# Kernel optimization log

Measured on AMD Instinct MI355X. Metric: run time of the kernel, lower is better.

The kernel has to match this reference:

```python
import jax, jax.numpy as jnp
import numpy as np

R0 = 1.0
DIM_A, DIM_V, DIM_D = 32, 32, 32
N_NODES = 20000
N_EDGES = 640000


def radial_encode_8(r, r0):
    # 8 Gaussian radial basis functions on the edge length |r_ij|
    d = jnp.linalg.norm(r, axis=-1)                      # [E]
    centers = jnp.linspace(0.0, r0, 8)                   # [8]
    width = r0 / 8.0
    return jnp.exp(-(((d[..., None] - centers) / width) ** 2))  # [E,8]


def tens_sigmoid_vec(v):
    # norm-saturating nonlinearity for rank-1 tensors (direction-preserving)
    n2 = jnp.sum(v * v, axis=-1, keepdims=True)
    return v * jax.lax.rsqrt(1.0 + n2)


def setup_inputs() -> dict:
    key = jax.random.key(0)
    ks = jax.random.split(key, 12)

    def lin(k, fan_in, fan_out):
        return jax.random.normal(k, (fan_in, fan_out), jnp.float32) / np.float32(np.sqrt(fan_in))

    return dict(
        r_ij=jax.random.normal(ks[0], (N_EDGES, 3), jnp.float32),
        w_rad=lin(ks[1], 8, DIM_A), b_rad=jnp.zeros((DIM_A,), jnp.float32),
        w_direct=lin(ks[2], DIM_A, DIM_A),
        w1=lin(ks[3], DIM_A, 2 * DIM_A), b1=jnp.zeros((2 * DIM_A,), jnp.float32),
        w2=lin(ks[4], 2 * DIM_A, 2 * DIM_A), b2=jnp.zeros((2 * DIM_A,), jnp.float32),
        w3=lin(ks[5], 2 * DIM_A, DIM_A), b3=jnp.zeros((DIM_A,), jnp.float32),
        w_v=lin(ks[6], DIM_A, DIM_V),
        w_d=lin(ks[7], DIM_A, DIM_D),
        edges_src=jax.random.randint(ks[8], (N_EDGES,), 0, N_NODES),
        n_nodes=N_NODES,
    )


def reference(r_ij, w_rad, b_rad, w_direct, w1, b1, w2, b2, w3, b3, w_v, w_d,
              edges_src, n_nodes):
    lrelu = lambda x: jnp.where(x > 0, x, 0.1 * x)
    # radial MLP: Linear(8, a) -> MLP (lin_direct + 3-layer leakyrelu net)
    h = radial_encode_8(r_ij, R0) @ w_rad + b_rad                      # [E,a]
    rad = h @ w_direct + (lrelu(lrelu(h @ w1 + b1) @ w2 + b2) @ w3 + b3)  # [E,a]
    rs = tens_sigmoid_vec(r_ij * (7.0 / R0))                            # [E,3]

    seg = lambda x: jax.ops.segment_sum(x, edges_src, num_segments=n_nodes)
    A_a = seg(rad)                                                      # [N,a]
    A_v = seg(rad[:, :, None] * rs[:, None, :])                         # [N,a,3]
    # phi_d_ij = rad ⊗ rs ⊗ rs per edge  -> [E,a,3,3], then scatter-sum
    A_d = seg(rad[:, :, None, None] * rs[:, None, None, :] * rs[:, None, :, None])  # [N,a,3,3]

    out_v = jnp.einsum('nac,av->nvc', A_v, w_v)                         # TensLinear rank 1
    out_d = jnp.einsum('naij,ad->ndij', A_d, w_d)                       # TensLinear rank 2
    return A_a, out_v, out_d
```

## Files before the change

### kernel.cpp

```cpp
#include <hip/hip_runtime.h>
#include <hip/hip_bf16.h>
#include <hip/hip_fp16.h>
#include <math.h>


#define TSIZE 8192
#define DMAX  2.0f
#define EPB   4
#define NPB   4
#define ROWB  512
#define ROWF  128

#define O_WRAD 0
#define O_BRAD 256
#define O_WDIR 288
#define O_W1   1312
#define O_B1   3360
#define O_W2   3424
#define O_B2   7520
#define O_W3   7584
#define O_B3   9632
#define O_WV   9664
#define O_WD   10688
#define W_TOT  11712

typedef float        f32x4 __attribute__((ext_vector_type(4)));
typedef unsigned int u32x2 __attribute__((ext_vector_type(2)));

struct TE { float r, v, d; };

__device__ __forceinline__ float lrelu(float x) { return x > 0.0f ? x : 0.1f * x; }

__device__ __forceinline__ float ldf(const void* p, int i, bool f32) {
    return f32 ? ((const float*)p)[i]
               : __uint_as_float(((unsigned int)((const unsigned short*)p)[i]) << 16);
}
__device__ __forceinline__ void stf(void* p, size_t i, float v, bool f32) {
    if (f32) ((float*)p)[i] = v;
    else     ((__hip_bfloat16*)p)[i] = __float2bfloat16(v);
}

__device__ __forceinline__ bool detect_f32(const void* r) {
    const unsigned short* p = (const unsigned short*)r;
    int bad = 0;
#pragma unroll 8
    for (int i = 0; i < 128; i++) {
        float v = __uint_as_float(((unsigned int)p[i]) << 16);
        bad |= (!isfinite(v) || fabsf(v) > 1e5f) ? 1 : 0;
    }
    return bad != 0;
}

__device__ __forceinline__ void load8x16(
    const void* p0, const void* p1, const void* p2, const void* p3,
    const void* p4, const void* p5, const void* p6, const void* p7,
    f32x4& q0, f32x4& q1, f32x4& q2, f32x4& q3,
    f32x4& q4, f32x4& q5, f32x4& q6, f32x4& q7) {
    asm volatile(
        "global_load_dwordx4 %0, %8, off\n\t"
        "global_load_dwordx4 %1, %9, off\n\t"
        "global_load_dwordx4 %2, %10, off\n\t"
        "global_load_dwordx4 %3, %11, off\n\t"
        "global_load_dwordx4 %4, %12, off\n\t"
        "global_load_dwordx4 %5, %13, off\n\t"
        "global_load_dwordx4 %6, %14, off\n\t"
        "global_load_dwordx4 %7, %15, off\n\t"
        "s_waitcnt vmcnt(0)"
        : "=&v"(q0), "=&v"(q1), "=&v"(q2), "=&v"(q3),
          "=&v"(q4), "=&v"(q5), "=&v"(q6), "=&v"(q7)
        : "v"(p0), "v"(p1), "v"(p2), "v"(p3),
          "v"(p4), "v"(p5), "v"(p6), "v"(p7));
}

__global__ void __launch_bounds__(256) k_prep(
    const void* __restrict__ r_ij,
    const void* w_rad, const void* b_rad, const void* w_direct,
    const void* w1, const void* b1, const void* w2, const void* b2,
    const void* w3, const void* b3, const void* w_v, const void* w_d,
    float* __restrict__ wcat, int* __restrict__ flag,
    int* __restrict__ counts, int N) {
    const int b = blockIdx.x;
    if (b == 0) {
        if (threadIdx.x == 0) flag[0] = detect_f32(r_ij) ? 1 : 0;
    } else if (b <= 11) {
        const bool f32 = detect_f32(r_ij);
        const void* src; int cnt; int off;
        switch (b) {
            case 1:  src = w_rad;    cnt = 256;  off = O_WRAD; break;
            case 2:  src = b_rad;    cnt = 32;   off = O_BRAD; break;
            case 3:  src = w_direct; cnt = 1024; off = O_WDIR; break;
            case 4:  src = w1;       cnt = 2048; off = O_W1;   break;
            case 5:  src = b1;       cnt = 64;   off = O_B1;   break;
            case 6:  src = w2;       cnt = 4096; off = O_W2;   break;
            case 7:  src = b2;       cnt = 64;   off = O_B2;   break;
            case 8:  src = w3;       cnt = 2048; off = O_W3;   break;
            case 9:  src = b3;       cnt = 32;   off = O_B3;   break;
            case 10: src = w_v;      cnt = 1024; off = O_WV;   break;
            default: src = w_d;      cnt = 1024; off = O_WD;   break;
        }
        for (int i = threadIdx.x; i < cnt; i += 256)
            wcat[off + i] = ldf(src, i, f32);
    } else {
        const int i = (b - 12) * 256 + threadIdx.x;
        if (i < N) counts[i] = 0;
    }
}

__global__ void __launch_bounds__(64 * EPB) k_tabrank(
    const float* __restrict__ wcat, float* __restrict__ tabI,
    const int* __restrict__ src, int* __restrict__ counts,
    unsigned short* __restrict__ rank, int E) {
    __shared__ float Lh[EPB][32], Lt1[EPB][64], Lt2[EPB][64], Lrad[EPB][32];

    const int TB = TSIZE / EPB;
    if (blockIdx.x >= TB) {
        const int e = (blockIdx.x - TB) * 256 + threadIdx.x;
        if (e < E) rank[e] = (unsigned short)atomicAdd(&counts[src[e]], 1);
        return;
    }

    const int s = threadIdx.x >> 6;
    const int j = threadIdx.x & 63;
    const int e = blockIdx.x * EPB + s;
    const float d = (float)e * (DMAX / (float)(TSIZE - 1));

    float enc[8];
#pragma unroll
    for (int k = 0; k < 8; k++) {
        float t = (d - (float)k * (1.0f / 7.0f)) * 8.0f;
        enc[k] = expf(-t * t);
    }

    if (j < 32) {
        float hv = wcat[O_BRAD + j];
#pragma unroll
        for (int k = 0; k < 8; k++) hv = fmaf(enc[k], wcat[O_WRAD + k * 32 + j], hv);
        Lh[s][j] = hv;
    }
    __syncthreads();

    {
        float v = wcat[O_B1 + j];
#pragma unroll
        for (int i = 0; i < 32; i++) v = fmaf(Lh[s][i], wcat[O_W1 + i * 64 + j], v);
        Lt1[s][j] = lrelu(v);
    }
    __syncthreads();

    {
        float v = wcat[O_B2 + j];
#pragma unroll
        for (int i = 0; i < 64; i++) v = fmaf(Lt1[s][i], wcat[O_W2 + i * 64 + j], v);
        Lt2[s][j] = lrelu(v);
    }
    __syncthreads();

    if (j < 32) {
        float v = wcat[O_B3 + j];
#pragma unroll
        for (int i = 0; i < 64; i++) v = fmaf(Lt2[s][i], wcat[O_W3 + i * 32 + j], v);
#pragma unroll
        for (int i = 0; i < 32; i++) v = fmaf(Lh[s][i], wcat[O_WDIR + i * 32 + j], v);
        Lrad[s][j] = v;
    }
    __syncthreads();

    if (j < 32) {
        float sv = 0.0f, sd = 0.0f;
#pragma unroll
        for (int i = 0; i < 32; i++) {
            float ri = Lrad[s][i];
            sv = fmaf(ri, wcat[O_WV + i * 32 + j], sv);
            sd = fmaf(ri, wcat[O_WD + i * 32 + j], sd);
        }
        float* row = tabI + (size_t)e * ROWF + j * 4;
        row[0] = Lrad[s][j];
        row[1] = sv;
        row[2] = sd;
        row[3] = 0.0f;
    }
}

__global__ void __launch_bounds__(1024) k_scan(const int* __restrict__ counts,
                                               int* __restrict__ rowstart,
                                               int N, int E) {
    __shared__ int part[1024];
    const int t = threadIdx.x;
    const int CH = (N + 1023) / 1024;
    const int lo = t * CH;
    const int hi = min(lo + CH, N);
    int s = 0;
    for (int i = lo; i < hi; i++) s += counts[i];
    part[t] = s;
    __syncthreads();
    for (int off = 1; off < 1024; off <<= 1) {
        int v = part[t];
        int w = (t >= off) ? part[t - off] : 0;
        __syncthreads();
        part[t] = v + w;
        __syncthreads();
    }
    int run = (t == 0) ? 0 : part[t - 1];
    for (int i = lo; i < hi; i++) { rowstart[i] = run; run += counts[i]; }
    if (t == 0) rowstart[N] = E;
}

template <bool P16>
__global__ void __launch_bounds__(256) k_place2(
        const int* __restrict__ src, const unsigned short* __restrict__ rank,
        const int* __restrict__ rowstart, const void* __restrict__ r_ij,
        const int* __restrict__ flag, void* __restrict__ epsv, int E) {
    const bool f32 = flag[0] != 0;
    const int e = blockIdx.x * 256 + threadIdx.x;
    if (e >= E) return;
    const int pos = rowstart[src[e]] + (int)rank[e];
    const float x = ldf(r_ij, 3 * e + 0, f32);
    const float y = ldf(r_ij, 3 * e + 1, f32);
    const float z = ldf(r_ij, 3 * e + 2, f32);
    const float d2 = x * x + y * y + z * z;
    const float inv = rsqrtf(1.0f + 49.0f * d2);
    const float u = fminf(sqrtf(d2), DMAX) * ((float)(TSIZE - 1) / DMAX);
    const int ti = (int)(u + 0.5f);
    const float rs0 = 7.0f * x * inv, rs1 = 7.0f * y * inv, rs2 = 7.0f * z * inv;
    if (P16) {
        ((float4*)epsv)[pos] =
            make_float4(rs0, rs1, rs2, __int_as_float(ti * ROWB));
    } else {
        const unsigned int h0 = __half_as_ushort(__float2half(rs0));
        const unsigned int h1 = __half_as_ushort(__float2half(rs1));
        const unsigned int h2 = __half_as_ushort(__float2half(rs2));
        ((uint2*)epsv)[pos] =
            make_uint2(h0 | (h1 << 16), h2 | ((unsigned)ti << 16));
    }
}

#define ACC16(Q, U)                                                           \
    do {                                                                      \
        const float x = (Q).x, y = (Q).y, z = (Q).z;                          \
        accA += (U).x;                                                        \
        v0 += (U).y * x; v1 += (U).y * y; v2 += (U).y * z;                    \
        const float _tx = (U).z * x, _ty = (U).z * y, _tz = (U).z * z;        \
        d00 += _tx * x; d01 += _tx * y; d02 += _tx * z;                       \
        d10 += _ty * x; d11 += _ty * y; d12 += _ty * z;                       \
        d20 += _tz * x; d21 += _tz * y; d22 += _tz * z;                       \
    } while (0)

template <bool P16>
__global__ void __launch_bounds__(64 * NPB, 4) k_nodes2(
    const void* __restrict__ epsv,
    const int* __restrict__ rowstart,
    const float* __restrict__ tabI,
    const int* __restrict__ flag,
    void* __restrict__ out, int N) {
    const int wave = threadIdx.x >> 6;
    const int lane = threadIdx.x & 63;
    const int n0 = (blockIdx.x * NPB + wave) * 2;
    const int a = lane & 31;
    const int half = lane >> 5;
    const int myn = n0 + half;
    const bool f32 = flag[0] != 0;
    const char* tabA = (const char*)tabI + a * 16;

    int s0 = 0, s1 = 0;
    if (myn < N) { s0 = rowstart[myn]; s1 = rowstart[myn + 1]; }
    const int mylen = s1 - s0;
    const int lenA = __shfl(mylen, 0);
    const int lenB = __shfl(mylen, 32);
    const int minl = min(lenA, lenB);
    const int maxl = max(lenA, lenB);
    const int mclamp = max(mylen - 1, 0);

    float accA = 0.f, v0 = 0.f, v1 = 0.f, v2 = 0.f;
    float d00 = 0.f, d01 = 0.f, d02 = 0.f,
          d10 = 0.f, d11 = 0.f, d12 = 0.f,
          d20 = 0.f, d21 = 0.f, d22 = 0.f;

    if (P16) {
        int i = 0;
        for (; i + 8 <= minl; i += 8) {
            const char* pb = (const char*)epsv + (size_t)(s0 + i) * 16;
            f32x4 q0, q1, q2, q3, q4, q5, q6, q7;
            load8x16(pb, pb + 16, pb + 32, pb + 48,
                     pb + 64, pb + 80, pb + 96, pb + 112,
                     q0, q1, q2, q3, q4, q5, q6, q7);
            f32x4 u0, u1, u2, u3, u4, u5, u6, u7;
            load8x16(tabA + __float_as_int(q0.w), tabA + __float_as_int(q1.w),
                     tabA + __float_as_int(q2.w), tabA + __float_as_int(q3.w),
                     tabA + __float_as_int(q4.w), tabA + __float_as_int(q5.w),
                     tabA + __float_as_int(q6.w), tabA + __float_as_int(q7.w),
                     u0, u1, u2, u3, u4, u5, u6, u7);
            ACC16(q0, u0); ACC16(q1, u1); ACC16(q2, u2); ACC16(q3, u3);
            ACC16(q4, u4); ACC16(q5, u5); ACC16(q6, u6); ACC16(q7, u7);
        }
        for (; i < maxl; i += 8) {
            float m0, m1, m2, m3, m4, m5, m6, m7;
#define TIDX(K) ((i + K) < mylen ? (i + K) : mclamp)
#define TPTR(K) ((const char*)epsv + (size_t)(s0 + TIDX(K)) * 16)
            m0 = (i + 0 < mylen) ? 1.f : 0.f;
            m1 = (i + 1 < mylen) ? 1.f : 0.f;
            m2 = (i + 2 < mylen) ? 1.f : 0.f;
            m3 = (i + 3 < mylen) ? 1.f : 0.f;
            m4 = (i + 4 < mylen) ? 1.f : 0.f;
            m5 = (i + 5 < mylen) ? 1.f : 0.f;
            m6 = (i + 6 < mylen) ? 1.f : 0.f;
            m7 = (i + 7 < mylen) ? 1.f : 0.f;
            f32x4 q0, q1, q2, q3, q4, q5, q6, q7;
            load8x16(TPTR(0), TPTR(1), TPTR(2), TPTR(3),
                     TPTR(4), TPTR(5), TPTR(6), TPTR(7),
                     q0, q1, q2, q3, q4, q5, q6, q7);
#undef TPTR
#undef TIDX
            f32x4 u0, u1, u2, u3, u4, u5, u6, u7;
            load8x16(tabA + __float_as_int(q0.w), tabA + __float_as_int(q1.w),
                     tabA + __float_as_int(q2.w), tabA + __float_as_int(q3.w),
                     tabA + __float_as_int(q4.w), tabA + __float_as_int(q5.w),
                     tabA + __float_as_int(q6.w), tabA + __float_as_int(q7.w),
                     u0, u1, u2, u3, u4, u5, u6, u7);
#define SAPX(K)                                                               \
            do { f32x4 uu = u##K; uu.x *= m##K; uu.y *= m##K; uu.z *= m##K;   \
                 ACC16(q##K, uu); } while (0)
            SAPX(0); SAPX(1); SAPX(2); SAPX(3);
            SAPX(4); SAPX(5); SAPX(6); SAPX(7);
#undef SAPX
        }
    } else {
        for (int i = 0; i < maxl; i++) {
            if (i < mylen) {
                const u32x2 qh = *((const u32x2*)epsv + (s0 + i));
                const float x = __half2float(__ushort_as_half(
                    (unsigned short)(qh.x & 0xffffu)));
                const float y = __half2float(__ushort_as_half(
                    (unsigned short)(qh.x >> 16)));
                const float z = __half2float(__ushort_as_half(
                    (unsigned short)(qh.y & 0xffffu)));
                const TE t = *(const TE*)(tabA + (int)(qh.y >> 16) * ROWB);
                accA += t.r;
                v0 += t.v * x; v1 += t.v * y; v2 += t.v * z;
                const float _tx = t.d * x, _ty = t.d * y, _tz = t.d * z;
                d00 += _tx * x; d01 += _tx * y; d02 += _tx * z;
                d10 += _ty * x; d11 += _ty * y; d12 += _ty * z;
                d20 += _tz * x; d21 += _tz * y; d22 += _tz * z;
            }
        }
    }

    if (myn >= N) return;
    const size_t baseV = (size_t)N * 32;
    const size_t baseD = (size_t)N * 128;
    stf(out, (size_t)myn * 32 + a, accA, f32);
    const size_t vb = baseV + (size_t)myn * 96 + a * 3;
    stf(out, vb + 0, v0, f32);
    stf(out, vb + 1, v1, f32);
    stf(out, vb + 2, v2, f32);
    const size_t db = baseD + (size_t)myn * 288 + a * 9;
    stf(out, db + 0, d00, f32);
    stf(out, db + 1, d01, f32);
    stf(out, db + 2, d02, f32);
    stf(out, db + 3, d10, f32);
    stf(out, db + 4, d11, f32);
    stf(out, db + 5, d12, f32);
    stf(out, db + 6, d20, f32);
    stf(out, db + 7, d21, f32);
    stf(out, db + 8, d22, f32);
}

__global__ void __launch_bounds__(256) k_place_g(
        const int* __restrict__ src, const unsigned short* __restrict__ rank,
        const int* __restrict__ rowstart, int* __restrict__ perm, int E) {
    const int e = blockIdx.x * 256 + threadIdx.x;
    if (e < E) perm[rowstart[src[e]] + (int)rank[e]] = e;
}
__global__ void __launch_bounds__(256) k_nodes_fb(
    const int* __restrict__ perm, const void* __restrict__ r_ij,
    const int* __restrict__ rowstart, const float* __restrict__ tabI,
    const int* __restrict__ flag, void* __restrict__ out, int N) {
    const int wave = threadIdx.x >> 6;
    const int lane = threadIdx.x & 63;
    const int n = blockIdx.x * 4 + wave;
    if (n >= N) return;
    const int a = lane & 31;
    const bool hi = (lane >> 5) != 0;
    const bool f32 = flag[0] != 0;
    const int s0 = rowstart[n], s1 = rowstart[n + 1];
    float accR = 0.f, acc1 = 0.f, acc2 = 0.f, acc3 = 0.f,
          acc4 = 0.f, acc5 = 0.f, acc6 = 0.f;
    for (int idx = s0; idx < s1; idx++) {
        const int e = perm[idx];
        const float x0 = ldf(r_ij, 3 * e + 0, f32);
        const float y0 = ldf(r_ij, 3 * e + 1, f32);
        const float z0 = ldf(r_ij, 3 * e + 2, f32);
        const float d2 = x0 * x0 + y0 * y0 + z0 * z0;
        const float inv = rsqrtf(1.0f + 49.0f * d2);
        const float x = 7.0f * x0 * inv, y = 7.0f * y0 * inv, z = 7.0f * z0 * inv;
        const float u = fminf(sqrtf(d2), DMAX) * ((float)(TSIZE - 1) / DMAX);
        const int b = (int)(u + 0.5f) * ROWF + a * 4;
        const float ra = tabI[b], rv = tabI[b + 1], rd = tabI[b + 2];
        const float b1 = (hi ? rd : rv) * (hi ? y : 1.0f);
        const float b2 = rd * (hi ? z : x);
        accR += ra;
        acc1 += b1 * x; acc2 += b1 * y; acc3 += b1 * z;
        acc4 += b2 * x; acc5 += b2 * y; acc6 += b2 * z;
    }
    const size_t baseV = (size_t)N * 32;
    const size_t baseD = (size_t)N * 128;
    if (!hi) {
        stf(out, (size_t)n * 32 + a, accR, f32);
        const size_t vb = baseV + (size_t)n * 96 + a * 3;
        stf(out, vb + 0, acc1, f32);
        stf(out, vb + 1, acc2, f32);
        stf(out, vb + 2, acc3, f32);
        const size_t db = baseD + (size_t)n * 288 + a * 9;
        stf(out, db + 0, acc4, f32);
        stf(out, db + 1, acc5, f32);
        stf(out, db + 2, acc6, f32);
    } else {
        const size_t db = baseD + (size_t)n * 288 + a * 9;
        stf(out, db + 3, acc1, f32);
        stf(out, db + 4, acc2, f32);
        stf(out, db + 5, acc3, f32);
        stf(out, db + 6, acc4, f32);
        stf(out, db + 7, acc5, f32);
        stf(out, db + 8, acc6, f32);
    }
}

extern "C" void kernel_launch(void* const* d_in, const int* in_sizes, int n_in,
                              void* d_out, int out_size, void* d_ws, size_t ws_size,
                              hipStream_t stream) {
    const void* r_ij     = d_in[0];
    const void* w_rad    = d_in[1];
    const void* b_rad    = d_in[2];
    const void* w_direct = d_in[3];
    const void* w1       = d_in[4];
    const void* b1       = d_in[5];
    const void* w2       = d_in[6];
    const void* b2       = d_in[7];
    const void* w3       = d_in[8];
    const void* b3       = d_in[9];
    const void* w_v      = d_in[10];
    const void* w_d      = d_in[11];
    const int* edges_src = (const int*)d_in[12];

    const int E = in_sizes[12];
    const int N = out_size / 416;
    const int TB = TSIZE / EPB;
    const int ZB = (N + 255) / 256;
    const int EB = (E + 255) / 256;
    const int nodeBlocks = (N + 2 * NPB - 1) / (2 * NPB);

    const size_t tailBytes = ((size_t)W_TOT + 1) * 4 + (size_t)TSIZE * ROWF * 4
                           + ((size_t)N + N + 1) * 4 + (size_t)E * 2 + 64;
    const bool p16 = ws_size >= (size_t)E * 16 + tailBytes;
    const bool p8  = !p16 && ws_size >= (size_t)E * 8 + tailBytes;

    char* w = (char*)d_ws;
    if (p16 || p8) {
        const size_t slot = (size_t)E * (p16 ? 16 : 8);
        void* eps      = (void*)w;
        float* wcat    = (float*)(w + slot);
        int* flag      = (int*)(wcat + W_TOT);
        float* tabI    = (float*)(flag + 1);
        int* counts    = (int*)(tabI + (size_t)TSIZE * ROWF);
        int* rowstart  = counts + N;
        unsigned short* rank = (unsigned short*)(rowstart + N + 1);

        k_prep<<<12 + ZB, 256, 0, stream>>>(
            r_ij, w_rad, b_rad, w_direct, w1, b1, w2, b2, w3, b3, w_v, w_d,
            wcat, flag, counts, N);
        k_tabrank<<<TB + EB, 64 * EPB, 0, stream>>>(
            wcat, tabI, edges_src, counts, rank, E);
        k_scan<<<1, 1024, 0, stream>>>(counts, rowstart, N, E);
        if (p16) {
            k_place2<true><<<EB, 256, 0, stream>>>(
                edges_src, rank, rowstart, r_ij, flag, eps, E);
            k_nodes2<true><<<nodeBlocks, 64 * NPB, 0, stream>>>(
                eps, rowstart, tabI, flag, d_out, N);
        } else {
            k_place2<false><<<EB, 256, 0, stream>>>(
                edges_src, rank, rowstart, r_ij, flag, eps, E);
            k_nodes2<false><<<nodeBlocks, 64 * NPB, 0, stream>>>(
                eps, rowstart, tabI, flag, d_out, N);
        }
    } else {
        int* perm      = (int*)w;
        float* wcat    = (float*)(w + (size_t)E * 4);
        int* flag      = (int*)(wcat + W_TOT);
        float* tabI    = (float*)(flag + 1);
        int* counts    = (int*)(tabI + (size_t)TSIZE * ROWF);
        int* rowstart  = counts + N;
        unsigned short* rank = (unsigned short*)(rowstart + N + 1);

        k_prep<<<12 + ZB, 256, 0, stream>>>(
            r_ij, w_rad, b_rad, w_direct, w1, b1, w2, b2, w3, b3, w_v, w_d,
            wcat, flag, counts, N);
        k_tabrank<<<TB + EB, 64 * EPB, 0, stream>>>(
            wcat, tabI, edges_src, counts, rank, E);
        k_scan<<<1, 1024, 0, stream>>>(counts, rowstart, N, E);
        k_place_g<<<EB, 256, 0, stream>>>(edges_src, rank, rowstart, perm, E);
        k_nodes_fb<<<(N + 3) / 4, 256, 0, stream>>>(
            perm, r_ij, rowstart, tabI, flag, d_out, N);
    }
}
```

Measured before the change: 211.7 us.

## Software-pipeline edge/table loads in node kernel and parallelize row-start scan

The node accumulation loop now double-buffers the per-edge payload loads: the next batch of 8 edge records is fetched while the table gather for the current batch is in flight. Partial vmcnt waits replace the full drain, hiding gather latency. This adds registers, so launch bounds drop from 4 to 3 waves per EU. The single-block 1024-thread scan is replaced by a two-kernel scheme (per-64 block sums, then per-block prefix with a wave scan), trading an extra launch for parallelism. The table is aligned to 16 bytes.

```diff
diff --git a/kernel.cpp b/kernel.cpp
--- a/kernel.cpp
+++ b/kernel.cpp
@@ -70,6 +70,41 @@
           "=&v"(q4), "=&v"(q5), "=&v"(q6), "=&v"(q7)
         : "v"(p0), "v"(p1), "v"(p2), "v"(p3),
           "v"(p4), "v"(p5), "v"(p6), "v"(p7));
+}
+
+__device__ __forceinline__ void load8x16_nw(
+    const void* p0, const void* p1, const void* p2, const void* p3,
+    const void* p4, const void* p5, const void* p6, const void* p7,
+    f32x4& q0, f32x4& q1, f32x4& q2, f32x4& q3,
+    f32x4& q4, f32x4& q5, f32x4& q6, f32x4& q7) {
+    asm volatile(
+        "global_load_dwordx4 %0, %8, off\n\t"
+        "global_load_dwordx4 %1, %9, off\n\t"
+        "global_load_dwordx4 %2, %10, off\n\t"
+        "global_load_dwordx4 %3, %11, off\n\t"
+        "global_load_dwordx4 %4, %12, off\n\t"
+        "global_load_dwordx4 %5, %13, off\n\t"
+        "global_load_dwordx4 %6, %14, off\n\t"
+        "global_load_dwordx4 %7, %15, off"
+        : "=&v"(q0), "=&v"(q1), "=&v"(q2), "=&v"(q3),
+          "=&v"(q4), "=&v"(q5), "=&v"(q6), "=&v"(q7)
+        : "v"(p0), "v"(p1), "v"(p2), "v"(p3),
+          "v"(p4), "v"(p5), "v"(p6), "v"(p7));
+}
+
+__device__ __forceinline__ void waitv8(
+    f32x4& r0, f32x4& r1, f32x4& r2, f32x4& r3,
+    f32x4& r4, f32x4& r5, f32x4& r6, f32x4& r7) {
+    asm volatile("s_waitcnt vmcnt(8)"
+        : "+v"(r0), "+v"(r1), "+v"(r2), "+v"(r3),
+          "+v"(r4), "+v"(r5), "+v"(r6), "+v"(r7));
+}
+__device__ __forceinline__ void waitv0(
+    f32x4& r0, f32x4& r1, f32x4& r2, f32x4& r3,
+    f32x4& r4, f32x4& r5, f32x4& r6, f32x4& r7) {
+    asm volatile("s_waitcnt vmcnt(0)"
+        : "+v"(r0), "+v"(r1), "+v"(r2), "+v"(r3),
+          "+v"(r4), "+v"(r5), "+v"(r6), "+v"(r7));
 }
 
 __global__ void __launch_bounds__(256) k_prep(
@@ -181,28 +216,34 @@
     }
 }
 
-__global__ void __launch_bounds__(1024) k_scan(const int* __restrict__ counts,
-                                               int* __restrict__ rowstart,
-                                               int N, int E) {
-    __shared__ int part[1024];
-    const int t = threadIdx.x;
-    const int CH = (N + 1023) / 1024;
-    const int lo = t * CH;
-    const int hi = min(lo + CH, N);
-    int s = 0;
-    for (int i = lo; i < hi; i++) s += counts[i];
-    part[t] = s;
-    __syncthreads();
-    for (int off = 1; off < 1024; off <<= 1) {
-        int v = part[t];
-        int w = (t >= off) ? part[t - off] : 0;
-        __syncthreads();
-        part[t] = v + w;
-        __syncthreads();
-    }
-    int run = (t == 0) ? 0 : part[t - 1];
-    for (int i = lo; i < hi; i++) { rowstart[i] = run; run += counts[i]; }
-    if (t == 0) rowstart[N] = E;
+__global__ void __launch_bounds__(64) k_sum(const int* __restrict__ counts,
+                                            int* __restrict__ coarse, int N) {
+    const int lane = threadIdx.x;
+    const int n = blockIdx.x * 64 + lane;
+    int s = (n < N) ? counts[n] : 0;
+    for (int off = 32; off > 0; off >>= 1) s += __shfl_down(s, off);
+    if (lane == 0) coarse[blockIdx.x] = s;
+}
+
+__global__ void __launch_bounds__(64) k_scan2c(const int* __restrict__ counts,
+                                               const int* __restrict__ coarse,
+                                               int* __restrict__ rowstart, int N) {
+    const int lane = threadIdx.x;
+    const int b = blockIdx.x;
+    int cp = 0;
+    for (int j = lane; j < b; j += 64) cp += coarse[j];
+    for (int off = 32; off > 0; off >>= 1) cp += __shfl_down(cp, off);
+    const int cpre = __shfl(cp, 0);
+
+    const int n = b * 64 + lane;
+    const int v = (n < N) ? counts[n] : 0;
+    int inc = v;
+    for (int off = 1; off < 64; off <<= 1) {
+        int y = __shfl_up(inc, off);
+        if (lane >= off) inc += y;
+    }
+    if (n < N) rowstart[n] = cpre + inc - v;
+    if (n == N - 1) rowstart[N] = cpre + inc;
 }
 
 template <bool P16>
@@ -245,8 +286,29 @@
         d20 += _tz * x; d21 += _tz * y; d22 += _tz * z;                       \
     } while (0)
 
+#define P8ARGS(R) R##0, R##1, R##2, R##3, R##4, R##5, R##6, R##7
+#define LOADP_NW(R, IDX)                                                      \
+    do { const char* _pp = (const char*)epsv + (size_t)(IDX) * 16;            \
+         load8x16_nw(_pp, _pp + 16, _pp + 32, _pp + 48,                       \
+                     _pp + 64, _pp + 80, _pp + 96, _pp + 112, P8ARGS(R));     \
+    } while (0)
+#define LOADT_NW(R, Q)                                                        \
+    load8x16_nw(tabA + __float_as_int((Q##0).w),                              \
+                tabA + __float_as_int((Q##1).w),                              \
+                tabA + __float_as_int((Q##2).w),                              \
+                tabA + __float_as_int((Q##3).w),                              \
+                tabA + __float_as_int((Q##4).w),                              \
+                tabA + __float_as_int((Q##5).w),                              \
+                tabA + __float_as_int((Q##6).w),                              \
+                tabA + __float_as_int((Q##7).w),                              \
+                P8ARGS(R))
+#define ACCB(Q, T)                                                            \
+    do { ACC16(Q##0, T##0); ACC16(Q##1, T##1); ACC16(Q##2, T##2);             \
+         ACC16(Q##3, T##3); ACC16(Q##4, T##4); ACC16(Q##5, T##5);             \
+         ACC16(Q##6, T##6); ACC16(Q##7, T##7); } while (0)
+
 template <bool P16>
-__global__ void __launch_bounds__(64 * NPB, 4) k_nodes2(
+__global__ void __launch_bounds__(64 * NPB, 3) k_nodes2(
     const void* __restrict__ epsv,
     const int* __restrict__ rowstart,
     const float* __restrict__ tabI,
@@ -277,20 +339,40 @@
 
     if (P16) {
         int i = 0;
-        for (; i + 8 <= minl; i += 8) {
-            const char* pb = (const char*)epsv + (size_t)(s0 + i) * 16;
-            f32x4 q0, q1, q2, q3, q4, q5, q6, q7;
-            load8x16(pb, pb + 16, pb + 32, pb + 48,
-                     pb + 64, pb + 80, pb + 96, pb + 112,
-                     q0, q1, q2, q3, q4, q5, q6, q7);
-            f32x4 u0, u1, u2, u3, u4, u5, u6, u7;
-            load8x16(tabA + __float_as_int(q0.w), tabA + __float_as_int(q1.w),
-                     tabA + __float_as_int(q2.w), tabA + __float_as_int(q3.w),
-                     tabA + __float_as_int(q4.w), tabA + __float_as_int(q5.w),
-                     tabA + __float_as_int(q6.w), tabA + __float_as_int(q7.w),
-                     u0, u1, u2, u3, u4, u5, u6, u7);
-            ACC16(q0, u0); ACC16(q1, u1); ACC16(q2, u2); ACC16(q3, u3);
-            ACC16(q4, u4); ACC16(q5, u5); ACC16(q6, u6); ACC16(q7, u7);
+        if (minl >= 8) {
+            f32x4 pa0, pa1, pa2, pa3, pa4, pa5, pa6, pa7;
+            f32x4 pb0, pb1, pb2, pb3, pb4, pb5, pb6, pb7;
+            f32x4 tt0, tt1, tt2, tt3, tt4, tt5, tt6, tt7;
+            LOADP_NW(pa, s0);
+            waitv0(P8ARGS(pa));
+            for (; i + 24 <= minl; i += 16) {
+                LOADT_NW(tt, pa);
+                LOADP_NW(pb, s0 + i + 8);
+                waitv8(P8ARGS(tt));
+                ACCB(pa, tt);
+                waitv0(P8ARGS(pb));
+                LOADT_NW(tt, pb);
+                LOADP_NW(pa, s0 + i + 16);
+                waitv8(P8ARGS(tt));
+                ACCB(pb, tt);
+                waitv0(P8ARGS(pa));
+            }
+            if (i + 16 <= minl) {
+                LOADT_NW(tt, pa);
+                LOADP_NW(pb, s0 + i + 8);
+                waitv8(P8ARGS(tt));
+                ACCB(pa, tt);
+                waitv0(P8ARGS(pb));
+                LOADT_NW(tt, pb);
+                waitv0(P8ARGS(tt));
+                ACCB(pb, tt);
+                i += 16;
+            } else {
+                LOADT_NW(tt, pa);
+                waitv0(P8ARGS(tt));
+                ACCB(pa, tt);
+                i += 8;
+            }
         }
         for (; i < maxl; i += 8) {
             float m0, m1, m2, m3, m4, m5, m6, m7;
@@ -446,10 +528,11 @@
     const int TB = TSIZE / EPB;
     const int ZB = (N + 255) / 256;
     const int EB = (E + 255) / 256;
+    const int NB = (N + 63) / 64;
     const int nodeBlocks = (N + 2 * NPB - 1) / (2 * NPB);
 
-    const size_t tailBytes = ((size_t)W_TOT + 1) * 4 + (size_t)TSIZE * ROWF * 4
-                           + ((size_t)N + N + 1) * 4 + (size_t)E * 2 + 64;
+    const size_t tailBytes = ((size_t)W_TOT + 4) * 4 + (size_t)TSIZE * ROWF * 4
+                           + ((size_t)N + N + 1 + NB) * 4 + (size_t)E * 2 + 64;
     const bool p16 = ws_size >= (size_t)E * 16 + tailBytes;
     const bool p8  = !p16 && ws_size >= (size_t)E * 8 + tailBytes;
 
@@ -459,17 +542,19 @@
         void* eps      = (void*)w;
         float* wcat    = (float*)(w + slot);
         int* flag      = (int*)(wcat + W_TOT);
-        float* tabI    = (float*)(flag + 1);
+        float* tabI    = (float*)(flag + 4);
         int* counts    = (int*)(tabI + (size_t)TSIZE * ROWF);
         int* rowstart  = counts + N;
-        unsigned short* rank = (unsigned short*)(rowstart + N + 1);
+        int* coarse    = rowstart + N + 1;
+        unsigned short* rank = (unsigned short*)(coarse + NB);
 
         k_prep<<<12 + ZB, 256, 0, stream>>>(
             r_ij, w_rad, b_rad, w_direct, w1, b1, w2, b2, w3, b3, w_v, w_d,
             wcat, flag, counts, N);
         k_tabrank<<<TB + EB, 64 * EPB, 0, stream>>>(
             wcat, tabI, edges_src, counts, rank, E);
-        k_scan<<<1, 1024, 0, stream>>>(counts, rowstart, N, E);
+        k_sum<<<NB, 64, 0, stream>>>(counts, coarse, N);
+        k_scan2c<<<NB, 64, 0, stream>>>(counts, coarse, rowstart, N);
         if (p16) {
             k_place2<true><<<EB, 256, 0, stream>>>(
                 edges_src, rank, rowstart, r_ij, flag, eps, E);
@@ -485,17 +570,19 @@
         int* perm      = (int*)w;
         float* wcat    = (float*)(w + (size_t)E * 4);
         int* flag      = (int*)(wcat + W_TOT);
-        float* tabI    = (float*)(flag + 1);
+        float* tabI    = (float*)(flag + 4);
         int* counts    = (int*)(tabI + (size_t)TSIZE * ROWF);
         int* rowstart  = counts + N;
-        unsigned short* rank = (unsigned short*)(rowstart + N + 1);
+        int* coarse    = rowstart + N + 1;
+        unsigned short* rank = (unsigned short*)(coarse + NB);
 
         k_prep<<<12 + ZB, 256, 0, stream>>>(
             r_ij, w_rad, b_rad, w_direct, w1, b1, w2, b2, w3, b3, w_v, w_d,
             wcat, flag, counts, N);
         k_tabrank<<<TB + EB, 64 * EPB, 0, stream>>>(
             wcat, tabI, edges_src, counts, rank, E);
-        k_scan<<<1, 1024, 0, stream>>>(counts, rowstart, N, E);
+        k_sum<<<NB, 64, 0, stream>>>(counts, coarse, N);
+        k_scan2c<<<NB, 64, 0, stream>>>(counts, coarse, rowstart, N);
         k_place_g<<<EB, 256, 0, stream>>>(edges_src, rank, rowstart, perm, E);
         k_nodes_fb<<<(N + 3) / 4, 256, 0, stream>>>(
             perm, r_ij, rowstart, tabI, flag, d_out, N);
```

Measured after the change: 191.8 us. -9.4%, faster.
